# Performance work log

Measured on AMD Instinct MI355X. Metric: run time of the kernel, lower is better.

Reference implementation:

```python
import jax, jax.numpy as jnp
import numpy as np

N_X = 50000      # real nodes
N_MOTIF = 10000  # motif nodes
N = N_X + N_MOTIF
E = 1_920_000    # edges (avg degree 32)
NFEAT = 512
NHID = 256
PAD_N = 65536


def setup_inputs() -> dict:
    key = jax.random.key(0)
    ks = jax.random.split(key, 12)
    x = jax.random.normal(ks[0], (N_X, NFEAT), dtype=jnp.float32)
    motif_emb = jax.random.normal(ks[1], (N_MOTIF, NFEAT), dtype=jnp.float32)
    adj_rows = jax.random.randint(ks[2], (E,), 0, N)
    adj_cols = jax.random.randint(ks[3], (E,), 0, N)
    adj_vals = jax.random.uniform(ks[4], (E,), dtype=jnp.float32)
    # unique scatter positions (torch output[pos_idx]=x with distinct indices)
    pos_idx = jax.random.permutation(ks[5], PAD_N)[:N_X]
    # GraphConvolution params (pygcn style: support = x@W; out = spmm(adj, support) + b)
    s1 = 1.0 / np.sqrt(NHID)
    w1 = jax.random.uniform(ks[6], (NFEAT, NHID), minval=-s1, maxval=s1, dtype=jnp.float32)
    b1 = jax.random.uniform(ks[7], (NHID,), minval=-s1, maxval=s1, dtype=jnp.float32)
    w2 = jax.random.uniform(ks[8], (NHID, NHID), minval=-s1, maxval=s1, dtype=jnp.float32)
    b2 = jax.random.uniform(ks[9], (NHID,), minval=-s1, maxval=s1, dtype=jnp.float32)
    w3 = jax.random.uniform(ks[10], (NHID, NHID), minval=-s1, maxval=s1, dtype=jnp.float32)
    b3 = jax.random.uniform(ks[11], (NHID,), minval=-s1, maxval=s1, dtype=jnp.float32)
    return {"x": x, "motif_emb": motif_emb, "adj_rows": adj_rows, "adj_cols": adj_cols,
            "adj_vals": adj_vals, "pos_idx": pos_idx, "pad_n": PAD_N,
            "w1": w1, "b1": b1, "w2": w2, "b2": b2, "w3": w3, "b3": b3}


def _gcn_layer(h, rows, cols, vals, w, b):
    support = h @ w                                   # [N, nhid]
    msgs = vals[:, None] * support[cols]              # [E, nhid]
    agg = jax.ops.segment_sum(msgs, rows, num_segments=N)  # spmm(adj, support)
    return jax.nn.relu(agg + b)


def reference(x, motif_emb, adj_rows, adj_cols, adj_vals, pos_idx, pad_n,
              w1, b1, w2, b2, w3, b3):
    h = jnp.concatenate((x, motif_emb), axis=0)       # [N, nfeat]
    h = _gcn_layer(h, adj_rows, adj_cols, adj_vals, w1, b1)
    # dropout is identity in eval mode
    h = _gcn_layer(h, adj_rows, adj_cols, adj_vals, w2, b2)
    h = _gcn_layer(h, adj_rows, adj_cols, adj_vals, w3, b3)
    h = h[:N_X]                                       # drop motif nodes
    output = jnp.zeros((pad_n, h.shape[1]), dtype=h.dtype)
    output = output.at[pos_idx].set(h)                # irregular scatter-assign
    return output
```

## Files before the change

### kernel.cpp

```cpp
#include <hip/hip_runtime.h>

#define N_TOTAL 60000
#define N_X     50000
#define N_EDGE  1920000
#define NFEAT   512
#define NHID    256
#define SLOTS   96
#define NCHUNK  8

typedef __attribute__((ext_vector_type(8))) short bf16x8;
typedef __attribute__((ext_vector_type(4))) float f32x4;
typedef __attribute__((ext_vector_type(4))) unsigned u32x4;

__device__ __forceinline__ unsigned short f2bf(float f) {
    unsigned u = __float_as_uint(f);
    unsigned r = (u + 0x7FFFu + ((u >> 16) & 1u)) >> 16;
    return (unsigned short)r;
}
__device__ __forceinline__ float bf_lo(unsigned u) { return __uint_as_float(u << 16); }
__device__ __forceinline__ float bf_hi(unsigned u) { return __uint_as_float(u & 0xFFFF0000u); }

__global__ __launch_bounds__(256)
void cvt_w_all_kernel(const float* __restrict__ w1, const float* __restrict__ w2,
                      const float* __restrict__ w3, short* __restrict__ w1T,
                      short* __restrict__ w2T, short* __restrict__ w3T)
{
    int n = blockIdx.x;
    for (int k = threadIdx.x; k < NFEAT; k += 256)
        w1T[(size_t)n * NFEAT + k] = (short)f2bf(w1[(size_t)k * NHID + n]);
    for (int k = threadIdx.x; k < NHID; k += 256)
        w2T[(size_t)n * NHID + k] = (short)f2bf(w2[(size_t)k * NHID + n]);
    for (int k = threadIdx.x; k < NHID; k += 256)
        w3T[(size_t)n * NHID + k] = (short)f2bf(w3[(size_t)k * NHID + n]);
}

#define LDA 40

template<bool AF32>
__global__ __launch_bounds__(256)
void gemm_bt_kernel(const float* __restrict__ Af, const float* __restrict__ A2f, int split,
                    const short* __restrict__ Ab, const short* __restrict__ BT,
                    short* __restrict__ C, int M, int K)
{
    __shared__ short As[128 * LDA];
    __shared__ short Bs[128 * LDA];
    const int t    = threadIdx.x;
    const int lane = t & 63;
    const int wave = t >> 6;
    const int wm   = wave & 1;
    const int wn   = wave >> 1;
    const int l16  = lane & 15;
    const int quad = lane >> 4;
    const int bm   = blockIdx.x * 128;
    const int bn   = blockIdx.y * 128;

    f32x4 acc[4][4] = {};

    const int srow = t >> 2;
    const int sch  = t & 3;
    const int frow = t >> 1;
    const int fh   = t & 1;

    for (int kk = 0; kk < K; kk += 32) {
        if (AF32) {
            int row = bm + frow;
            float4 v0 = {}, v1 = {}, v2 = {}, v3 = {};
            if (row < M) {
                const float* src = (row < split) ? (Af + (size_t)row * K)
                                                 : (A2f + (size_t)(row - split) * K);
                const float4* p = (const float4*)(src + kk + fh * 16);
                v0 = p[0]; v1 = p[1]; v2 = p[2]; v3 = p[3];
            }
            short* dst = &As[frow * LDA + fh * 16];
            short tmp[16] = {
                (short)f2bf(v0.x), (short)f2bf(v0.y), (short)f2bf(v0.z), (short)f2bf(v0.w),
                (short)f2bf(v1.x), (short)f2bf(v1.y), (short)f2bf(v1.z), (short)f2bf(v1.w),
                (short)f2bf(v2.x), (short)f2bf(v2.y), (short)f2bf(v2.z), (short)f2bf(v2.w),
                (short)f2bf(v3.x), (short)f2bf(v3.y), (short)f2bf(v3.z), (short)f2bf(v3.w)};
            *(bf16x8*)(dst)     = *(const bf16x8*)&tmp[0];
            *(bf16x8*)(dst + 8) = *(const bf16x8*)&tmp[8];
        } else {
            bf16x8 va0 = {}, va1 = {};
            int r0 = bm + srow, r1 = bm + srow + 64;
            if (r0 < M) va0 = *(const bf16x8*)(Ab + (size_t)r0 * K + kk + sch * 8);
            if (r1 < M) va1 = *(const bf16x8*)(Ab + (size_t)r1 * K + kk + sch * 8);
            *(bf16x8*)&As[srow * LDA + sch * 8]        = va0;
            *(bf16x8*)&As[(srow + 64) * LDA + sch * 8] = va1;
        }
        {
            bf16x8 vb0 = *(const bf16x8*)(BT + (size_t)(bn + srow) * K + kk + sch * 8);
            bf16x8 vb1 = *(const bf16x8*)(BT + (size_t)(bn + srow + 64) * K + kk + sch * 8);
            *(bf16x8*)&Bs[srow * LDA + sch * 8]        = vb0;
            *(bf16x8*)&Bs[(srow + 64) * LDA + sch * 8] = vb1;
        }
        __syncthreads();

        bf16x8 af[4], bfr[4];
        #pragma unroll
        for (int i = 0; i < 4; i++) {
            af[i]  = *(const bf16x8*)&As[(wm * 64 + i * 16 + l16) * LDA + quad * 8];
            bfr[i] = *(const bf16x8*)&Bs[(wn * 64 + i * 16 + l16) * LDA + quad * 8];
        }
        #pragma unroll
        for (int i = 0; i < 4; i++)
            #pragma unroll
            for (int j = 0; j < 4; j++)
                acc[i][j] = __builtin_amdgcn_mfma_f32_16x16x32_bf16(af[i], bfr[j], acc[i][j], 0, 0, 0);
        __syncthreads();
    }

    #pragma unroll
    for (int i = 0; i < 4; i++) {
        #pragma unroll
        for (int r = 0; r < 4; r++) {
            int row = bm + wm * 64 + i * 16 + quad * 4 + r;
            if (row < M) {
                #pragma unroll
                for (int j = 0; j < 4; j++) {
                    int col = bn + wn * 64 + j * 16 + l16;
                    size_t idx = (size_t)(col >> 5) * M * 32 + (size_t)row * 32 + (col & 31);
                    __builtin_nontemporal_store((short)f2bf(acc[i][j][r]), C + idx);
                }
            }
        }
    }
}

__global__ __launch_bounds__(256)
void init_cursor_kernel(int* __restrict__ cursor)
{
    int i = blockIdx.x * 256 + threadIdx.x;
    if (i < N_TOTAL) cursor[i] = i * SLOTS;
}

__global__ __launch_bounds__(256)
void scatter_edges_kernel(const int* __restrict__ rows, const int* __restrict__ cols,
                          const float* __restrict__ vals, int* __restrict__ cursor,
                          unsigned* __restrict__ edges)
{
    const int b = blockIdx.x;
    const int g = b & 7;
    const int i = (b >> 3) * 256 + threadIdx.x;
    const int lo = g * (N_TOTAL / 8);
    const int hi = lo + (N_TOTAL / 8);
    int r = __builtin_nontemporal_load(&rows[i]);
    if (r >= lo && r < hi) {
        unsigned rec = (unsigned)cols[i] | ((unsigned)f2bf(vals[i]) << 16);
        int p = atomicAdd(&cursor[r], 1);
        edges[p] = rec;
    }
}

template<int MODE>
__global__ __launch_bounds__(256)
void spmm_relu_kernel(const int* __restrict__ row_end, const unsigned* __restrict__ edges,
                      const u32x4* __restrict__ supportC, const float* __restrict__ bias,
                      u32x4* __restrict__ out_bf, float* __restrict__ out_f32,
                      const int* __restrict__ pos, int nrows)
{
    const int chunk = blockIdx.x & 7;
    const int grp   = blockIdx.x >> 3;
    const int wave  = threadIdx.x >> 6;
    const int lane  = threadIdx.x & 63;
    const int gid   = lane >> 2;
    const int fl    = lane & 3;
    const int rbase = grp * 64 + wave * 16;
    if (rbase >= nrows) return;
    const int r  = rbase + gid;
    const int rc = min(r, nrows - 1);
    const int start = rc * SLOTS;
    const int len   = row_end[rc] - start;
    const u32x4* __restrict__ sb = supportC + (size_t)chunk * N_TOTAL * 4 + fl;
    const u32x4* __restrict__ ep = (const u32x4*)(edges + start);

    float a[8] = {};
    u32x4 e0 = ep[0];
    u32x4 e1 = ep[1];
    for (int it = 0; it < len; it += 8) {
        const int g = it >> 2;
        u32x4 n0 = ep[g + 2];
        u32x4 n1 = ep[g + 3];
        #pragma unroll
        for (int s = 0; s < 4; s++) {
            unsigned es = e0[s];
            u32x4 u = sb[(size_t)(es & 0xFFFFu) * 4];
            float w = bf_hi(es);
            #pragma unroll
            for (int k = 0; k < 4; k++) {
                a[2*k]     += w * bf_lo(u[k]);
                a[2*k + 1] += w * bf_hi(u[k]);
            }
        }
        #pragma unroll
        for (int s = 0; s < 4; s++) {
            unsigned es = e1[s];
            u32x4 u = sb[(size_t)(es & 0xFFFFu) * 4];
            float w = bf_hi(es);
            #pragma unroll
            for (int k = 0; k < 4; k++) {
                a[2*k]     += w * bf_lo(u[k]);
                a[2*k + 1] += w * bf_hi(u[k]);
            }
        }
        e0 = n0; e1 = n1;
    }

    const f32x4* bb = (const f32x4*)bias + chunk * 8 + fl * 2;
    f32x4 bv0 = bb[0], bv1 = bb[1];
    float o[8];
    #pragma unroll
    for (int k = 0; k < 8; k++) {
        float bk = (k < 4) ? bv0[k] : bv1[k - 4];
        o[k] = fmaxf(a[k] + bk, 0.f);
    }
    if (r < nrows) {
        if (MODE == 1) {
            f32x4 q0 = {o[0], o[1], o[2], o[3]};
            f32x4 q1 = {o[4], o[5], o[6], o[7]};
            f32x4* dst = (f32x4*)out_f32 + (size_t)pos[r] * 64 + chunk * 8 + fl * 2;
            __builtin_nontemporal_store(q0, dst);
            __builtin_nontemporal_store(q1, dst + 1);
        } else {
            u32x4 q;
            #pragma unroll
            for (int k = 0; k < 4; k++)
                q[k] = (unsigned)f2bf(o[2*k]) | ((unsigned)f2bf(o[2*k + 1]) << 16);
            __builtin_nontemporal_store(q, out_bf + (size_t)r * 32 + chunk * 4 + fl);
        }
    }
}

extern "C" void kernel_launch(void* const* d_in, const int* in_sizes, int n_in,
                              void* d_out, int out_size, void* d_ws, size_t ws_size,
                              hipStream_t stream)
{
    const float* x     = (const float*)d_in[0];
    const float* motif = (const float*)d_in[1];
    const int*   rows  = (const int*)d_in[2];
    const int*   cols  = (const int*)d_in[3];
    const float* vals  = (const float*)d_in[4];
    const int*   pos   = (const int*)d_in[5];
    const float* w1 = (const float*)d_in[7];
    const float* b1 = (const float*)d_in[8];
    const float* w2 = (const float*)d_in[9];
    const float* b2 = (const float*)d_in[10];
    const float* w3 = (const float*)d_in[11];
    const float* b3 = (const float*)d_in[12];
    (void)ws_size; (void)n_in; (void)in_sizes;

    char* ws = (char*)d_ws;
    size_t off = 0;
    short* h_bf     = (short*)(ws + off); off += (size_t)N_TOTAL * NHID * 2;
    short* support  = (short*)(ws + off); off += (size_t)N_TOTAL * NHID * 2;
    short* w1T      = (short*)(ws + off); off += (size_t)NHID * NFEAT * 2;
    short* w2T      = (short*)(ws + off); off += (size_t)NHID * NHID * 2;
    short* w3T      = (short*)(ws + off); off += (size_t)NHID * NHID * 2;
    int* cursor     = (int*)(ws + off);   off += 60032 * 4;
    unsigned* edges = (unsigned*)(ws + off); off += (size_t)N_TOTAL * SLOTS * 4 + 256;

    hipMemsetAsync(d_out, 0, (size_t)out_size * sizeof(float), stream);
    hipMemsetAsync(edges, 0, (size_t)N_TOTAL * SLOTS * 4, stream);
    cvt_w_all_kernel<<<NHID, 256, 0, stream>>>(w1, w2, w3, w1T, w2T, w3T);
    init_cursor_kernel<<<(N_TOTAL + 255) / 256, 256, 0, stream>>>(cursor);
    scatter_edges_kernel<<<(N_EDGE / 256) * 8, 256, 0, stream>>>(rows, cols, vals, cursor, edges);

    dim3 ggrid((N_TOTAL + 127) / 128, NHID / 128);
    const int sgrid0 = ((N_TOTAL + 63) / 64) * NCHUNK;
    const int sgrid1 = ((N_X + 63) / 64) * NCHUNK;

    gemm_bt_kernel<true><<<ggrid, 256, 0, stream>>>(x, motif, N_X, nullptr, w1T, support, N_TOTAL, NFEAT);
    spmm_relu_kernel<0><<<sgrid0, 256, 0, stream>>>(cursor, edges, (const u32x4*)support, b1,
                                                    (u32x4*)h_bf, nullptr, nullptr, N_TOTAL);
    gemm_bt_kernel<false><<<ggrid, 256, 0, stream>>>(nullptr, nullptr, 0, h_bf, w2T, support, N_TOTAL, NHID);
    spmm_relu_kernel<0><<<sgrid0, 256, 0, stream>>>(cursor, edges, (const u32x4*)support, b2,
                                                    (u32x4*)h_bf, nullptr, nullptr, N_TOTAL);
    gemm_bt_kernel<false><<<ggrid, 256, 0, stream>>>(nullptr, nullptr, 0, h_bf, w3T, support, N_TOTAL, NHID);
    spmm_relu_kernel<1><<<sgrid1, 256, 0, stream>>>(cursor, edges, (const u32x4*)support, b3,
                                                    nullptr, (float*)d_out, pos, N_X);
}
```

Before: 702.4 us.

## Bind SpMM feature chunk to XCC id with persistent atomic work queue

The SpMM kernels become persistent: 2048 blocks each read their XCC id through s_getreg and use it as the feature chunk, so every XCC gathers only its own slice of the support matrix and keeps that slice in its local L2. Waves pull 16-row groups from a per-chunk atomic counter instead of a fixed grid mapping, which also balances uneven row lengths. This relies on there being exactly 8 XCCs and on blocks being spread evenly across them. If placement is uneven, some chunks finish late while others sit idle, and the per-group atomics add some contention.

```diff
diff --git a/kernel.cpp b/kernel.cpp
--- a/kernel.cpp
+++ b/kernel.cpp
@@ -127,10 +127,11 @@
 }
 
 __global__ __launch_bounds__(256)
-void init_cursor_kernel(int* __restrict__ cursor)
+void init_cursor_kernel(int* __restrict__ cursor, int* __restrict__ wctr)
 {
     int i = blockIdx.x * 256 + threadIdx.x;
     if (i < N_TOTAL) cursor[i] = i * SLOTS;
+    if (i < 32) wctr[i] = 0;
 }
 
 __global__ __launch_bounds__(256)
@@ -156,76 +157,83 @@
 void spmm_relu_kernel(const int* __restrict__ row_end, const unsigned* __restrict__ edges,
                       const u32x4* __restrict__ supportC, const float* __restrict__ bias,
                       u32x4* __restrict__ out_bf, float* __restrict__ out_f32,
-                      const int* __restrict__ pos, int nrows)
-{
-    const int chunk = blockIdx.x & 7;
-    const int grp   = blockIdx.x >> 3;
-    const int wave  = threadIdx.x >> 6;
+                      const int* __restrict__ pos, int nrows, int ngroups,
+                      int* __restrict__ wctr)
+{
+    int xcc;
+    asm volatile("s_getreg_b32 %0, hwreg(HW_REG_XCC_ID)" : "=s"(xcc));
+    const int chunk = xcc & 7;
     const int lane  = threadIdx.x & 63;
     const int gid   = lane >> 2;
     const int fl    = lane & 3;
-    const int rbase = grp * 64 + wave * 16;
-    if (rbase >= nrows) return;
-    const int r  = rbase + gid;
-    const int rc = min(r, nrows - 1);
-    const int start = rc * SLOTS;
-    const int len   = row_end[rc] - start;
     const u32x4* __restrict__ sb = supportC + (size_t)chunk * N_TOTAL * 4 + fl;
-    const u32x4* __restrict__ ep = (const u32x4*)(edges + start);
-
-    float a[8] = {};
-    u32x4 e0 = ep[0];
-    u32x4 e1 = ep[1];
-    for (int it = 0; it < len; it += 8) {
-        const int g = it >> 2;
-        u32x4 n0 = ep[g + 2];
-        u32x4 n1 = ep[g + 3];
-        #pragma unroll
-        for (int s = 0; s < 4; s++) {
-            unsigned es = e0[s];
-            u32x4 u = sb[(size_t)(es & 0xFFFFu) * 4];
-            float w = bf_hi(es);
+    const f32x4* bb = (const f32x4*)bias + chunk * 8 + fl * 2;
+    const f32x4 bv0 = bb[0], bv1 = bb[1];
+
+    for (;;) {
+        int g;
+        if (lane == 0) g = atomicAdd(&wctr[chunk], 1);
+        g = __builtin_amdgcn_readfirstlane(g);
+        if (g >= ngroups) break;
+
+        const int r  = g * 16 + gid;
+        const int rc = min(r, nrows - 1);
+        const int start = rc * SLOTS;
+        const int len   = row_end[rc] - start;
+        const u32x4* __restrict__ ep = (const u32x4*)(edges + start);
+
+        float a[8] = {};
+        u32x4 e0 = ep[0];
+        u32x4 e1 = ep[1];
+        for (int it = 0; it < len; it += 8) {
+            const int gq = it >> 2;
+            u32x4 n0 = ep[gq + 2];
+            u32x4 n1 = ep[gq + 3];
             #pragma unroll
-            for (int k = 0; k < 4; k++) {
-                a[2*k]     += w * bf_lo(u[k]);
-                a[2*k + 1] += w * bf_hi(u[k]);
-            }
-        }
-        #pragma unroll
-        for (int s = 0; s < 4; s++) {
-            unsigned es = e1[s];
-            u32x4 u = sb[(size_t)(es & 0xFFFFu) * 4];
-            float w = bf_hi(es);
+            for (int s = 0; s < 4; s++) {
+                unsigned es = e0[s];
+                u32x4 u = sb[(size_t)(es & 0xFFFFu) * 4];
+                float w = bf_hi(es);
+                #pragma unroll
+                for (int k = 0; k < 4; k++) {
+                    a[2*k]     += w * bf_lo(u[k]);
+                    a[2*k + 1] += w * bf_hi(u[k]);
+                }
+            }
             #pragma unroll
-            for (int k = 0; k < 4; k++) {
-                a[2*k]     += w * bf_lo(u[k]);
-                a[2*k + 1] += w * bf_hi(u[k]);
-            }
-        }
-        e0 = n0; e1 = n1;
-    }
-
-    const f32x4* bb = (const f32x4*)bias + chunk * 8 + fl * 2;
-    f32x4 bv0 = bb[0], bv1 = bb[1];
-    float o[8];
-    #pragma unroll
-    for (int k = 0; k < 8; k++) {
-        float bk = (k < 4) ? bv0[k] : bv1[k - 4];
-        o[k] = fmaxf(a[k] + bk, 0.f);
-    }
-    if (r < nrows) {
-        if (MODE == 1) {
-            f32x4 q0 = {o[0], o[1], o[2], o[3]};
-            f32x4 q1 = {o[4], o[5], o[6], o[7]};
-            f32x4* dst = (f32x4*)out_f32 + (size_t)pos[r] * 64 + chunk * 8 + fl * 2;
-            __builtin_nontemporal_store(q0, dst);
-            __builtin_nontemporal_store(q1, dst + 1);
-        } else {
-            u32x4 q;
-            #pragma unroll
-            for (int k = 0; k < 4; k++)
-                q[k] = (unsigned)f2bf(o[2*k]) | ((unsigned)f2bf(o[2*k + 1]) << 16);
-            __builtin_nontemporal_store(q, out_bf + (size_t)r * 32 + chunk * 4 + fl);
+            for (int s = 0; s < 4; s++) {
+                unsigned es = e1[s];
+                u32x4 u = sb[(size_t)(es & 0xFFFFu) * 4];
+                float w = bf_hi(es);
+                #pragma unroll
+                for (int k = 0; k < 4; k++) {
+                    a[2*k]     += w * bf_lo(u[k]);
+                    a[2*k + 1] += w * bf_hi(u[k]);
+                }
+            }
+            e0 = n0; e1 = n1;
+        }
+
+        float o[8];
+        #pragma unroll
+        for (int k = 0; k < 8; k++) {
+            float bk = (k < 4) ? bv0[k] : bv1[k - 4];
+            o[k] = fmaxf(a[k] + bk, 0.f);
+        }
+        if (r < nrows) {
+            if (MODE == 1) {
+                f32x4 q0 = {o[0], o[1], o[2], o[3]};
+                f32x4 q1 = {o[4], o[5], o[6], o[7]};
+                f32x4* dst = (f32x4*)out_f32 + (size_t)pos[r] * 64 + chunk * 8 + fl * 2;
+                __builtin_nontemporal_store(q0, dst);
+                __builtin_nontemporal_store(q1, dst + 1);
+            } else {
+                u32x4 q;
+                #pragma unroll
+                for (int k = 0; k < 4; k++)
+                    q[k] = (unsigned)f2bf(o[2*k]) | ((unsigned)f2bf(o[2*k + 1]) << 16);
+                __builtin_nontemporal_store(q, out_bf + (size_t)r * 32 + chunk * 4 + fl);
+            }
         }
     }
 }
@@ -256,25 +264,27 @@
     short* w2T      = (short*)(ws + off); off += (size_t)NHID * NHID * 2;
     short* w3T      = (short*)(ws + off); off += (size_t)NHID * NHID * 2;
     int* cursor     = (int*)(ws + off);   off += 60032 * 4;
+    int* wctr       = (int*)(ws + off);   off += 32 * 4;
     unsigned* edges = (unsigned*)(ws + off); off += (size_t)N_TOTAL * SLOTS * 4 + 256;
 
     hipMemsetAsync(d_out, 0, (size_t)out_size * sizeof(float), stream);
-    hipMemsetAsync(edges, 0, (size_t)N_TOTAL * SLOTS * 4, stream);
+    hipMemsetAsync(edges, 0, (size_t)N_TOTAL * SLOTS * 4 + 256, stream);
     cvt_w_all_kernel<<<NHID, 256, 0, stream>>>(w1, w2, w3, w1T, w2T, w3T);
-    init_cursor_kernel<<<(N_TOTAL + 255) / 256, 256, 0, stream>>>(cursor);
+    init_cursor_kernel<<<(N_TOTAL + 255) / 256, 256, 0, stream>>>(cursor, wctr);
     scatter_edges_kernel<<<(N_EDGE / 256) * 8, 256, 0, stream>>>(rows, cols, vals, cursor, edges);
 
     dim3 ggrid((N_TOTAL + 127) / 128, NHID / 128);
-    const int sgrid0 = ((N_TOTAL + 63) / 64) * NCHUNK;
-    const int sgrid1 = ((N_X + 63) / 64) * NCHUNK;
+    const int PBLK = 2048;
+    const int ngrp0 = N_TOTAL / 16;
+    const int ngrp1 = N_X / 16;
 
     gemm_bt_kernel<true><<<ggrid, 256, 0, stream>>>(x, motif, N_X, nullptr, w1T, support, N_TOTAL, NFEAT);
-    spmm_relu_kernel<0><<<sgrid0, 256, 0, stream>>>(cursor, edges, (const u32x4*)support, b1,
-                                                    (u32x4*)h_bf, nullptr, nullptr, N_TOTAL);
+    spmm_relu_kernel<0><<<PBLK, 256, 0, stream>>>(cursor, edges, (const u32x4*)support, b1,
+                                                  (u32x4*)h_bf, nullptr, nullptr, N_TOTAL, ngrp0, wctr);
     gemm_bt_kernel<false><<<ggrid, 256, 0, stream>>>(nullptr, nullptr, 0, h_bf, w2T, support, N_TOTAL, NHID);
-    spmm_relu_kernel<0><<<sgrid0, 256, 0, stream>>>(cursor, edges, (const u32x4*)support, b2,
-                                                    (u32x4*)h_bf, nullptr, nullptr, N_TOTAL);
+    spmm_relu_kernel<0><<<PBLK, 256, 0, stream>>>(cursor, edges, (const u32x4*)support, b2,
+                                                  (u32x4*)h_bf, nullptr, nullptr, N_TOTAL, ngrp0, wctr + 8);
     gemm_bt_kernel<false><<<ggrid, 256, 0, stream>>>(nullptr, nullptr, 0, h_bf, w3T, support, N_TOTAL, NHID);
-    spmm_relu_kernel<1><<<sgrid1, 256, 0, stream>>>(cursor, edges, (const u32x4*)support, b3,
-                                                    nullptr, (float*)d_out, pos, N_X);
-}
+    spmm_relu_kernel<1><<<PBLK, 256, 0, stream>>>(cursor, edges, (const u32x4*)support, b3,
+                                                  nullptr, (float*)d_out, pos, N_X, ngrp1, wctr + 16);
+}
```

Measured after the change: 1.724 ms. +145.5%, slower.

## Restructure GEMM to stage only weights in LDS and load A fragments directly

Applied to the files above, without the earlier changes.

Replaces the shared-memory A/B tiled GEMM with a kernel that stages a 128-wide K slab of the weight matrix in LDS and has each wave load its A rows straight from global memory into MFMA fragments. Each wave now owns 32 rows by 128 columns instead of a 64x64 quadrant. The aim is to cut LDS traffic and the number of barriers per K step, since only weights go through LDS and barriers now happen once per 128 K. In exchange, A global loads are narrower, per-lane strided and not shared across waves, and there is little latency hiding between load and MFMA.

```diff
diff --git a/kernel.cpp b/kernel.cpp
--- a/kernel.cpp
+++ b/kernel.cpp
@@ -34,90 +34,84 @@
         w3T[(size_t)n * NHID + k] = (short)f2bf(w3[(size_t)k * NHID + n]);
 }
 
-#define LDA 40
+#define LDW 40
 
 template<bool AF32>
 __global__ __launch_bounds__(256)
-void gemm_bt_kernel(const float* __restrict__ Af, const float* __restrict__ A2f, int split,
-                    const short* __restrict__ Ab, const short* __restrict__ BT,
-                    short* __restrict__ C, int M, int K)
-{
-    __shared__ short As[128 * LDA];
-    __shared__ short Bs[128 * LDA];
-    const int t    = threadIdx.x;
-    const int lane = t & 63;
-    const int wave = t >> 6;
-    const int wm   = wave & 1;
-    const int wn   = wave >> 1;
-    const int l16  = lane & 15;
-    const int quad = lane >> 4;
-    const int bm   = blockIdx.x * 128;
-    const int bn   = blockIdx.y * 128;
-
-    f32x4 acc[4][4] = {};
-
-    const int srow = t >> 2;
-    const int sch  = t & 3;
-    const int frow = t >> 1;
-    const int fh   = t & 1;
-
-    for (int kk = 0; kk < K; kk += 32) {
-        if (AF32) {
-            int row = bm + frow;
-            float4 v0 = {}, v1 = {}, v2 = {}, v3 = {};
-            if (row < M) {
-                const float* src = (row < split) ? (Af + (size_t)row * K)
-                                                 : (A2f + (size_t)(row - split) * K);
-                const float4* p = (const float4*)(src + kk + fh * 16);
-                v0 = p[0]; v1 = p[1]; v2 = p[2]; v3 = p[3];
-            }
-            short* dst = &As[frow * LDA + fh * 16];
-            short tmp[16] = {
-                (short)f2bf(v0.x), (short)f2bf(v0.y), (short)f2bf(v0.z), (short)f2bf(v0.w),
-                (short)f2bf(v1.x), (short)f2bf(v1.y), (short)f2bf(v1.z), (short)f2bf(v1.w),
-                (short)f2bf(v2.x), (short)f2bf(v2.y), (short)f2bf(v2.z), (short)f2bf(v2.w),
-                (short)f2bf(v3.x), (short)f2bf(v3.y), (short)f2bf(v3.z), (short)f2bf(v3.w)};
-            *(bf16x8*)(dst)     = *(const bf16x8*)&tmp[0];
-            *(bf16x8*)(dst + 8) = *(const bf16x8*)&tmp[8];
-        } else {
-            bf16x8 va0 = {}, va1 = {};
-            int r0 = bm + srow, r1 = bm + srow + 64;
-            if (r0 < M) va0 = *(const bf16x8*)(Ab + (size_t)r0 * K + kk + sch * 8);
-            if (r1 < M) va1 = *(const bf16x8*)(Ab + (size_t)r1 * K + kk + sch * 8);
-            *(bf16x8*)&As[srow * LDA + sch * 8]        = va0;
-            *(bf16x8*)&As[(srow + 64) * LDA + sch * 8] = va1;
-        }
+void gemm_wlds_kernel(const float* __restrict__ Af, const float* __restrict__ A2f, int split,
+                      const short* __restrict__ Ab, const short* __restrict__ BT,
+                      short* __restrict__ C, int M, int K)
+{
+    __shared__ short Ws[4][128][LDW];
+    const int t     = threadIdx.x;
+    const int lane  = t & 63;
+    const int wave  = t >> 6;
+    const int l16   = lane & 15;
+    const int quad  = lane >> 4;
+    const int bm    = blockIdx.x * 128;
+    const int bn    = blockIdx.y * 128;
+    const int rowA0 = bm + wave * 32;
+
+    f32x4 acc[2][8] = {};
+
+    const int wn = t >> 1;
+    const int q2 = (t & 1) * 2;
+
+    for (int kh = 0; kh < K; kh += 128) {
+        __syncthreads();
         {
-            bf16x8 vb0 = *(const bf16x8*)(BT + (size_t)(bn + srow) * K + kk + sch * 8);
-            bf16x8 vb1 = *(const bf16x8*)(BT + (size_t)(bn + srow + 64) * K + kk + sch * 8);
-            *(bf16x8*)&Bs[srow * LDA + sch * 8]        = vb0;
-            *(bf16x8*)&Bs[(srow + 64) * LDA + sch * 8] = vb1;
+            const short* src = BT + (size_t)(bn + wn) * K + kh + q2 * 32;
+            #pragma unroll
+            for (int b = 0; b < 2; b++)
+                #pragma unroll
+                for (int v = 0; v < 4; v++)
+                    *(bf16x8*)&Ws[q2 + b][wn][v * 8] = *(const bf16x8*)(src + b * 32 + v * 8);
         }
         __syncthreads();
 
-        bf16x8 af[4], bfr[4];
-        #pragma unroll
-        for (int i = 0; i < 4; i++) {
-            af[i]  = *(const bf16x8*)&As[(wm * 64 + i * 16 + l16) * LDA + quad * 8];
-            bfr[i] = *(const bf16x8*)&Bs[(wn * 64 + i * 16 + l16) * LDA + quad * 8];
-        }
-        #pragma unroll
-        for (int i = 0; i < 4; i++)
-            #pragma unroll
-            for (int j = 0; j < 4; j++)
-                acc[i][j] = __builtin_amdgcn_mfma_f32_16x16x32_bf16(af[i], bfr[j], acc[i][j], 0, 0, 0);
-        __syncthreads();
+        #pragma unroll
+        for (int kb = 0; kb < 4; kb++) {
+            const int kk = kh + kb * 32;
+            bf16x8 af[2];
+            #pragma unroll
+            for (int i = 0; i < 2; i++) {
+                const int row = rowA0 + i * 16 + l16;
+                if (AF32) {
+                    float4 v0 = {}, v1 = {};
+                    if (row < M) {
+                        const float* s = (row < split) ? Af + (size_t)row * K
+                                                       : A2f + (size_t)(row - split) * K;
+                        const float4* p = (const float4*)(s + kk + quad * 8);
+                        v0 = p[0]; v1 = p[1];
+                    }
+                    short tmp[8] = {
+                        (short)f2bf(v0.x), (short)f2bf(v0.y), (short)f2bf(v0.z), (short)f2bf(v0.w),
+                        (short)f2bf(v1.x), (short)f2bf(v1.y), (short)f2bf(v1.z), (short)f2bf(v1.w)};
+                    af[i] = *(const bf16x8*)tmp;
+                } else {
+                    bf16x8 a = {};
+                    if (row < M) a = *(const bf16x8*)(Ab + (size_t)row * K + kk + quad * 8);
+                    af[i] = a;
+                }
+            }
+            #pragma unroll
+            for (int j = 0; j < 8; j++) {
+                bf16x8 bfr = *(const bf16x8*)&Ws[kb][j * 16 + l16][quad * 8];
+                acc[0][j] = __builtin_amdgcn_mfma_f32_16x16x32_bf16(af[0], bfr, acc[0][j], 0, 0, 0);
+                acc[1][j] = __builtin_amdgcn_mfma_f32_16x16x32_bf16(af[1], bfr, acc[1][j], 0, 0, 0);
+            }
+        }
     }
 
     #pragma unroll
-    for (int i = 0; i < 4; i++) {
+    for (int i = 0; i < 2; i++) {
         #pragma unroll
         for (int r = 0; r < 4; r++) {
-            int row = bm + wm * 64 + i * 16 + quad * 4 + r;
+            int row = rowA0 + i * 16 + quad * 4 + r;
             if (row < M) {
                 #pragma unroll
-                for (int j = 0; j < 4; j++) {
-                    int col = bn + wn * 64 + j * 16 + l16;
+                for (int j = 0; j < 8; j++) {
+                    int col = bn + j * 16 + l16;
                     size_t idx = (size_t)(col >> 5) * M * 32 + (size_t)row * 32 + (col & 31);
                     __builtin_nontemporal_store((short)f2bf(acc[i][j][r]), C + idx);
                 }
@@ -268,13 +262,13 @@
     const int sgrid0 = ((N_TOTAL + 63) / 64) * NCHUNK;
     const int sgrid1 = ((N_X + 63) / 64) * NCHUNK;
 
-    gemm_bt_kernel<true><<<ggrid, 256, 0, stream>>>(x, motif, N_X, nullptr, w1T, support, N_TOTAL, NFEAT);
+    gemm_wlds_kernel<true><<<ggrid, 256, 0, stream>>>(x, motif, N_X, nullptr, w1T, support, N_TOTAL, NFEAT);
     spmm_relu_kernel<0><<<sgrid0, 256, 0, stream>>>(cursor, edges, (const u32x4*)support, b1,
                                                     (u32x4*)h_bf, nullptr, nullptr, N_TOTAL);
-    gemm_bt_kernel<false><<<ggrid, 256, 0, stream>>>(nullptr, nullptr, 0, h_bf, w2T, support, N_TOTAL, NHID);
+    gemm_wlds_kernel<false><<<ggrid, 256, 0, stream>>>(nullptr, nullptr, 0, h_bf, w2T, support, N_TOTAL, NHID);
     spmm_relu_kernel<0><<<sgrid0, 256, 0, stream>>>(cursor, edges, (const u32x4*)support, b2,
                                                     (u32x4*)h_bf, nullptr, nullptr, N_TOTAL);
-    gemm_bt_kernel<false><<<ggrid, 256, 0, stream>>>(nullptr, nullptr, 0, h_bf, w3T, support, N_TOTAL, NHID);
+    gemm_wlds_kernel<false><<<ggrid, 256, 0, stream>>>(nullptr, nullptr, 0, h_bf, w3T, support, N_TOTAL, NHID);
     spmm_relu_kernel<1><<<sgrid1, 256, 0, stream>>>(cursor, edges, (const u32x4*)support, b3,
                                                     nullptr, (float*)d_out, pos, N_X);
 }
```

After: 755.8 us. 1.08x slower.
